# Kernel tuning notes

Hardware: AMD Instinct MI355X
Metric: run time of the kernel (lower is better)

The kernel has to match this reference:

```python
import jax, jax.numpy as jnp
import numpy as np

N, E, F, H = 20000, 320000, 128, 256   # nodes, edges, in-features, hidden
M, NQ = 4096, 2048                      # lsq rows, QP variables
LAMB_MAX = 2.0


def setup_inputs() -> dict:
    key = jax.random.key(0)
    ks = jax.random.split(key, 12)
    x = jax.random.normal(ks[0], (N, F), jnp.float32)
    edge_index = jax.random.randint(ks[1], (2, E), 0, N)
    A = jax.random.normal(ks[2], (M, NQ), jnp.float32) * 0.05
    b = jax.random.normal(ks[3], (M, 1), jnp.float32)
    feat_ids = jax.random.randint(ks[4], (NQ,), 0, N)
    x_prior = jax.random.uniform(ks[5], (NQ, 1), jnp.float32)
    lamb = jnp.ones((1,), jnp.float32)
    # ChebConv K=2 weights: one linear per Chebyshev order, plus bias
    W10 = jax.random.normal(ks[6], (F, H), jnp.float32) / np.sqrt(F)
    W11 = jax.random.normal(ks[7], (F, H), jnp.float32) / np.sqrt(F)
    b1 = jnp.zeros((H,), jnp.float32)
    W20 = jax.random.normal(ks[8], (H, 1), jnp.float32) / np.sqrt(H)
    W21 = jax.random.normal(ks[9], (H, 1), jnp.float32) / np.sqrt(H)
    b2 = jnp.zeros((1,), jnp.float32)
    return {"x": x, "edge_index": edge_index, "A": A, "b": b,
            "feat_ids": feat_ids, "x_prior": x_prior, "lamb": lamb,
            "W10": W10, "W11": W11, "b1": b1,
            "W20": W20, "W21": W21, "b2": b2}


def _cheb_conv(x, edge_index, W0, W1, bias, lam_max):
    """PyG ChebConv with K=2: out = x @ W0 + (2L/lam_max - I) x @ W1 + bias,
    L = I - D^{-1/2} A D^{-1/2}, via edge gather/scatter (no dense NxN)."""
    row, col = edge_index[0], edge_index[1]
    n = x.shape[0]
    deg = jax.ops.segment_sum(jnp.ones_like(row, dtype=x.dtype), row, num_segments=n)
    dinv = jnp.where(deg > 0, deg ** -0.5, 0.0)
    # normalized edge weight scaled by 2/lam_max, negated (off-diag of L_hat)
    w = -(2.0 / lam_max) * dinv[row] * dinv[col]              # [E]
    msg = jax.ops.segment_sum(w[:, None] * x[col], row, num_segments=n)
    Tx1 = msg + (2.0 / lam_max - 1.0) * x                      # diagonal of L_hat
    return x @ W0 + Tx1 @ W1 + bias


def reference(x, edge_index, A, b, feat_ids, x_prior, lamb,
              W10, W11, b1, W20, W21, b2):
    h = jax.nn.relu(_cheb_conv(x, edge_index, W10, W11, b1, LAMB_MAX))
    h = lamb[0] * jax.nn.relu(_cheb_conv(h, edge_index, W20, W21, b2, LAMB_MAX))
    hfold = h[feat_ids] + 1e-5                                 # [NQ, 1]
    q = hfold[:, 0]
    # QP: min 1/2 z^T Q z + p^T z with vacuous inequality (0*z <= 0.1) and no
    # equality constraints -> interior-point converges to unconstrained min.
    Q = A.T @ A + jnp.diag(q)                                  # [NQ, NQ]
    p = -(x_prior * hfold)[:, 0] - (b.T @ A)[0]                # [NQ]
    z = jnp.linalg.solve(Q, -p)                                # [NQ]
    return z[:, None]                                          # f.T -> [NQ, 1]
```

## Files before the change

kernel.cpp:

```cpp
#include <hip/hip_runtime.h>

#define N_NODES 20000
#define N_EDGES 320000
#define F_DIM   128
#define H_DIM   256
#define M_ROWS  4096
#define NQ      2048
#define NIT     18
#define MM_ROWS 20032

typedef __attribute__((ext_vector_type(8))) short short8;
typedef __attribute__((ext_vector_type(4))) float f32x4;


__device__ __forceinline__ float wred(float v) {
#pragma unroll
  for (int m = 32; m > 0; m >>= 1) v += __shfl_xor(v, m, 64);
  return v;
}

__device__ __forceinline__ float bred256(float v, float* lds) {
  v = wred(v);
  int w = threadIdx.x >> 6;
  if ((threadIdx.x & 63) == 0) lds[w] = v;
  __syncthreads();
  float tot = lds[0] + lds[1] + lds[2] + lds[3];
  __syncthreads();
  return tot;
}

__device__ __forceinline__ unsigned f2bf(float f) {
  unsigned u = __float_as_uint(f);
  unsigned r = u + 0x7fffu + ((u >> 16) & 1u);
  return r >> 16;
}
__device__ __forceinline__ float bflo(unsigned u) { return __uint_as_float(u << 16); }
__device__ __forceinline__ float bfhi(unsigned u) { return __uint_as_float(u & 0xffff0000u); }


__global__ __launch_bounds__(256) void k_deg(const int* __restrict__ ei, int* __restrict__ deg) {
  int e = blockIdx.x * 256 + threadIdx.x;
  if (e < N_EDGES) atomicAdd(&deg[ei[e]], 1);
}

__global__ __launch_bounds__(1024) void k_scan(const int* __restrict__ deg,
    int* __restrict__ rowstart, float* __restrict__ dinv) {
  __shared__ int part[1024];
  int t = threadIdx.x;
  const int chunk = (N_NODES + 1023) / 1024;
  int lo = t * chunk;
  int hi = lo + chunk; if (hi > N_NODES) hi = N_NODES;
  int s = 0;
  for (int i = lo; i < hi; ++i) {
    int d = deg[i];
    dinv[i] = d > 0 ? rsqrtf((float)d) : 0.f;
    s += d;
  }
  part[t] = s;
  __syncthreads();
  for (int off = 1; off < 1024; off <<= 1) {
    int v = part[t];
    int add = (t >= off) ? part[t - off] : 0;
    __syncthreads();
    part[t] = v + add;
    __syncthreads();
  }
  int base = (t > 0) ? part[t - 1] : 0;
  for (int i = lo; i < hi; ++i) { rowstart[i] = base; base += deg[i]; }
  if (t == 0) rowstart[N_NODES] = part[1023];
}

__global__ __launch_bounds__(256) void k_scatter(const int* __restrict__ ei,
    const int* __restrict__ rowstart, int* __restrict__ cursor,
    const float* __restrict__ dinv, int* __restrict__ cols, float* __restrict__ wvals) {
  int e = blockIdx.x * 256 + threadIdx.x;
  if (e >= N_EDGES) return;
  int r = ei[e];
  int c = ei[N_EDGES + e];
  int pos = rowstart[r] + atomicAdd(&cursor[r], 1);
  cols[pos] = c;
  wvals[pos] = -dinv[r] * dinv[c];
}

#define CONVX_BLKS (MM_ROWS * 16 / 256)

__global__ __launch_bounds__(256) void k_pack(const float* __restrict__ x,
    const float* __restrict__ W10, const float* __restrict__ W11,
    unsigned* __restrict__ xu, unsigned* __restrict__ Wtb) {
  int bx = blockIdx.x;
  if (bx < CONVX_BLKS) {
    int gid = bx * 256 + threadIdx.x;
    int row = gid >> 4;
    int q8 = gid & 15;
    uint4* xu4 = (uint4*)xu;
    if (row < N_NODES) {
      const float4* x4 = (const float4*)x;
      float4 a = x4[(size_t)row * 32 + q8 * 2];
      float4 b = x4[(size_t)row * 32 + q8 * 2 + 1];
      uint4 u;
      u.x = f2bf(a.x) | (f2bf(a.y) << 16);
      u.y = f2bf(a.z) | (f2bf(a.w) << 16);
      u.z = f2bf(b.x) | (f2bf(b.y) << 16);
      u.w = f2bf(b.z) | (f2bf(b.w) << 16);
      xu4[(size_t)row * 32 + q8] = u;
    } else {
      uint4 z = make_uint4(0, 0, 0, 0);
      xu4[(size_t)row * 32 + q8] = z;
      xu4[(size_t)row * 32 + 16 + q8] = z;
    }
  } else {
    int gid = (bx - CONVX_BLKS) * 256 + threadIdx.x;
    int n = gid >> 7;
    int u = gid & 127;
    int k0 = u * 2;
    float v0 = (k0 < 128) ? W10[(size_t)k0 * H_DIM + n]
                          : W11[(size_t)(k0 - 128) * H_DIM + n];
    float v1 = (k0 + 1 < 128) ? W10[(size_t)(k0 + 1) * H_DIM + n]
                              : W11[(size_t)(k0 - 127) * H_DIM + n];
    Wtb[(size_t)n * 128 + u] = f2bf(v0) | (f2bf(v1) << 16);
  }
}

__global__ __launch_bounds__(256) void k_msg1(const int* __restrict__ rowstart,
    const int* __restrict__ cols, const float* __restrict__ wvals,
    unsigned* __restrict__ xu) {
  int wid = (blockIdx.x * 256 + threadIdx.x) >> 6;
  int lane = threadIdx.x & 63;
  if (wid >= N_NODES) return;
  int s0 = rowstart[wid], s1 = rowstart[wid + 1];
  float2 acc = make_float2(0.f, 0.f);
  for (int e = s0; e < s1; ++e) {
    int c = cols[e];
    float w = wvals[e];
    unsigned u = xu[(size_t)c * 128 + lane];
    acc.x += w * bflo(u);
    acc.y += w * bfhi(u);
  }
  xu[(size_t)wid * 128 + 64 + lane] = f2bf(acc.x) | (f2bf(acc.y) << 16);
}

#define WS_ST 20

__global__ __launch_bounds__(256) void k_mm(const unsigned* __restrict__ xu,
    const unsigned* __restrict__ Wtb, const float* __restrict__ b1,
    const float* __restrict__ W20, const float* __restrict__ W21,
    float* __restrict__ t, float* __restrict__ s) {
  __shared__ unsigned Ws[2][256 * WS_ST];
  const int row0 = blockIdx.x * 64;
  const int tid = threadIdx.x;
  const int w = tid >> 6, lane = tid & 63;
  const int colb = w * 64;
  const int frow = lane & 15, fqo = (lane >> 4) * 4;
  const int c16 = lane & 15, q4 = lane >> 4;

  f32x4 acc[4][4];
#pragma unroll
  for (int a = 0; a < 4; ++a)
#pragma unroll
    for (int b = 0; b < 4; ++b) {
      acc[a][b][0] = 0.f; acc[a][b][1] = 0.f;
      acc[a][b][2] = 0.f; acc[a][b][3] = 0.f;
    }

  const uint4* Wtb4 = (const uint4*)Wtb;
  uint4 rw[4];
#pragma unroll
  for (int j = 0; j < 4; ++j) rw[j] = Wtb4[(size_t)tid * 32 + j];

  for (int kc = 0; kc < 8; ++kc) {
    const int b = kc & 1;
    unsigned* dst = Ws[b] + tid * WS_ST;
#pragma unroll
    for (int j = 0; j < 4; ++j) *(uint4*)(dst + j * 4) = rw[j];
    if (kc + 1 < 8) {
#pragma unroll
      for (int j = 0; j < 4; ++j) rw[j] = Wtb4[(size_t)tid * 32 + (kc + 1) * 4 + j];
    }
    __syncthreads();
    short8 af[4], bf[4];
#pragma unroll
    for (int a = 0; a < 4; ++a)
      af[a] = *(const short8*)(xu + (size_t)(row0 + a * 16 + frow) * 128 + kc * 16 + fqo);
#pragma unroll
    for (int n = 0; n < 4; ++n)
      bf[n] = *(const short8*)(Ws[b] + (colb + n * 16 + frow) * WS_ST + fqo);
#pragma unroll
    for (int a = 0; a < 4; ++a)
#pragma unroll
      for (int n = 0; n < 4; ++n)
        acc[a][n] = __builtin_amdgcn_mfma_f32_16x16x32_bf16(af[a], bf[n], acc[a][n], 0, 0, 0);
    __syncthreads();
  }

  float tp[4][4] = {}, sp[4][4] = {};
#pragma unroll
  for (int b2 = 0; b2 < 4; ++b2) {
    int gc = colb + b2 * 16 + c16;
    float w20 = W20[gc], w21 = W21[gc], bb = b1[gc];
#pragma unroll
    for (int a = 0; a < 4; ++a)
#pragma unroll
      for (int r = 0; r < 4; ++r) {
        float val = acc[a][b2][r] + bb;
        val = val > 0.f ? val : 0.f;
        tp[a][r] += val * w20;
        sp[a][r] += val * w21;
      }
  }
#pragma unroll
  for (int a = 0; a < 4; ++a)
#pragma unroll
    for (int r = 0; r < 4; ++r) {
#pragma unroll
      for (int m = 1; m < 16; m <<= 1) {
        tp[a][r] += __shfl_xor(tp[a][r], m, 64);
        sp[a][r] += __shfl_xor(sp[a][r], m, 64);
      }
    }
  if (c16 == 0) {
#pragma unroll
    for (int a = 0; a < 4; ++a)
#pragma unroll
      for (int r = 0; r < 4; ++r) {
        int gr = row0 + a * 16 + q4 * 4 + r;
        if (gr < N_NODES) {
          atomicAdd(&t[gr], tp[a][r]);
          atomicAdd(&s[gr], sp[a][r]);
        }
      }
  }
}


__global__ __launch_bounds__(256) void k_h2(const float* __restrict__ t,
    const float* __restrict__ s, const int* __restrict__ rowstart,
    const int* __restrict__ cols, const float* __restrict__ wvals,
    const float* __restrict__ lamb, const float* __restrict__ b2, float* __restrict__ h2) {
  int i = blockIdx.x * 256 + threadIdx.x;
  if (i >= N_NODES) return;
  float m = 0.f;
  int s0 = rowstart[i], s1 = rowstart[i + 1];
  for (int e = s0; e < s1; ++e) m += wvals[e] * s[cols[e]];
  float val = t[i] + m + b2[0];
  val = val > 0.f ? val : 0.f;
  h2[i] = lamb[0] * val;
}

__global__ __launch_bounds__(256) void k_prep(const float* __restrict__ A,
    const float* __restrict__ b, unsigned* __restrict__ Atu, float* __restrict__ btA_parts) {
  int jp = blockIdx.x * 256 + threadIdx.x;
  int k0 = blockIdx.y * 128;
  const float2* A2 = (const float2*)A;
  float acc0 = 0.f, acc1 = 0.f;
  for (int kk = 0; kk < 128; kk += 8) {
    float ax[8], ay[8];
#pragma unroll
    for (int i = 0; i < 8; ++i) {
      int k = k0 + kk + i;
      float2 a = A2[(size_t)k * 1024 + jp];
      float bk = b[k];
      acc0 += a.x * bk;
      acc1 += a.y * bk;
      ax[i] = a.x; ay[i] = a.y;
    }
    uint4 t0, t1;
    t0.x = f2bf(ax[0]) | (f2bf(ax[1]) << 16);
    t0.y = f2bf(ax[2]) | (f2bf(ax[3]) << 16);
    t0.z = f2bf(ax[4]) | (f2bf(ax[5]) << 16);
    t0.w = f2bf(ax[6]) | (f2bf(ax[7]) << 16);
    t1.x = f2bf(ay[0]) | (f2bf(ay[1]) << 16);
    t1.y = f2bf(ay[2]) | (f2bf(ay[3]) << 16);
    t1.z = f2bf(ay[4]) | (f2bf(ay[5]) << 16);
    t1.w = f2bf(ay[6]) | (f2bf(ay[7]) << 16);
    int uoff = (k0 + kk) >> 1;
    *(uint4*)(Atu + (size_t)(2 * jp) * 2048 + uoff) = t0;
    *(uint4*)(Atu + (size_t)(2 * jp + 1) * 2048 + uoff) = t1;
  }
  ((float2*)(btA_parts + (size_t)blockIdx.y * NQ))[jp] = make_float2(acc0, acc1);
}

__global__ __launch_bounds__(256) void k_qrhs(const float* __restrict__ h2,
    const int* __restrict__ feat_ids, const float* __restrict__ x_prior,
    const float* __restrict__ btA_parts, float* __restrict__ q, float* __restrict__ r) {
  int j = blockIdx.x * 256 + threadIdx.x;
  int f = feat_ids[j];
  float hf = h2[f] + 1e-5f;
  q[j] = hf;
  float bta = 0.f;
#pragma unroll
  for (int c = 0; c < 32; ++c) bta += btA_parts[(size_t)c * NQ + j];
  r[j] = x_prior[j] * hf + bta;
}

#define GR_ST 20
#define NTILE 136

__global__ __launch_bounds__(512) void k_gram(const unsigned* __restrict__ Atu,
                                              float* __restrict__ Gp) {
  __shared__ unsigned shmem[10240];
  int uu = blockIdx.x, bi = 0;
  while (uu >= 16 - bi) { uu -= 16 - bi; ++bi; }
  const int bj = bi + uu;
  const int i0 = bi * 128, j0 = bj * 128;
  const int kq = blockIdx.y;
  const int tid = threadIdx.x;
  const int grp = tid >> 8;
  const int t8 = tid & 255;
  const int w = tid >> 6;
  const int wt = w & 3;
  const int lane = tid & 63;
  const int wr = (wt >> 1) * 64, wc = (wt & 1) * 64;
  const int srow = t8 >> 1, suo = (t8 & 1) * 8;
  const int frow = lane & 15, fqo = (lane >> 4) * 4;

  unsigned* shA = shmem + grp * 5120;
  unsigned* shB = shA + 2560;

  f32x4 acc[4][4];
#pragma unroll
  for (int a = 0; a < 4; ++a)
#pragma unroll
    for (int b = 0; b < 4; ++b) {
      acc[a][b][0] = 0.f; acc[a][b][1] = 0.f;
      acc[a][b][2] = 0.f; acc[a][b][3] = 0.f;
    }

  const unsigned* pa = Atu + (size_t)(i0 + srow) * 2048 + kq * 512 + suo;
  const unsigned* pb = Atu + (size_t)(j0 + srow) * 2048 + kq * 512 + suo;

  int ku = grp * 16;
  uint4 ra0 = *(const uint4*)(pa + ku);
  uint4 ra1 = *(const uint4*)(pa + ku + 4);
  uint4 rb0 = *(const uint4*)(pb + ku);
  uint4 rb1 = *(const uint4*)(pb + ku + 4);

  for (int si = 0; si < 16; ++si) {
    unsigned* as = shA + srow * GR_ST + suo;
    unsigned* bs = shB + srow * GR_ST + suo;
    *(uint4*)as = ra0; *(uint4*)(as + 4) = ra1;
    *(uint4*)bs = rb0; *(uint4*)(bs + 4) = rb1;
    if (si + 1 < 16) {
      ku = (si + 1) * 32 + grp * 16;
      ra0 = *(const uint4*)(pa + ku);
      ra1 = *(const uint4*)(pa + ku + 4);
      rb0 = *(const uint4*)(pb + ku);
      rb1 = *(const uint4*)(pb + ku + 4);
    }
    __syncthreads();
    short8 af[4], bf[4];
#pragma unroll
    for (int a = 0; a < 4; ++a)
      af[a] = *(const short8*)(shA + (wr + a * 16 + frow) * GR_ST + fqo);
#pragma unroll
    for (int b2 = 0; b2 < 4; ++b2)
      bf[b2] = *(const short8*)(shB + (wc + b2 * 16 + frow) * GR_ST + fqo);
#pragma unroll
    for (int a = 0; a < 4; ++a)
#pragma unroll
      for (int b2 = 0; b2 < 4; ++b2)
        acc[a][b2] = __builtin_amdgcn_mfma_f32_16x16x32_bf16(af[a], bf[b2], acc[a][b2], 0, 0, 0);
    __syncthreads();
  }

  const int q4 = lane >> 4, c16 = lane & 15;
  float* comb = (float*)shmem;
#pragma unroll
  for (int rnd = 0; rnd < 2; ++rnd) {
    if (grp == 1 && (wt >> 1) == rnd) {
      float* dst = comb + (wt & 1) * 4160;
#pragma unroll
      for (int a = 0; a < 4; ++a)
#pragma unroll
        for (int b2 = 0; b2 < 4; ++b2)
#pragma unroll
          for (int r = 0; r < 4; ++r)
            dst[(a * 16 + q4 * 4 + r) * 65 + b2 * 16 + c16] = acc[a][b2][r];
    }
    __syncthreads();
    if (grp == 0 && (wt >> 1) == rnd) {
      const float* src = comb + (wt & 1) * 4160;
#pragma unroll
      for (int a = 0; a < 4; ++a)
#pragma unroll
        for (int b2 = 0; b2 < 4; ++b2)
#pragma unroll
          for (int r = 0; r < 4; ++r)
            acc[a][b2][r] += src[(a * 16 + q4 * 4 + r) * 65 + b2 * 16 + c16];
    }
    __syncthreads();
  }

  if (grp == 0) {
    float* Gz = Gp + ((size_t)kq * NTILE + blockIdx.x) * 16384;
#pragma unroll
    for (int a = 0; a < 4; ++a)
#pragma unroll
      for (int b2 = 0; b2 < 4; ++b2)
#pragma unroll
        for (int r = 0; r < 4; ++r) {
          int lr = wr + a * 16 + q4 * 4 + r;
          int lc = wc + b2 * 16 + c16;
          Gz[lr * 128 + lc] = acc[a][b2][r];
        }
  }
}

#define GT_ST 131

__global__ __launch_bounds__(256) void k_gconv(const float* __restrict__ Gp,
    const float* __restrict__ q, unsigned* __restrict__ Gb, float* __restrict__ qcorr) {
  __shared__ unsigned short T[128 * GT_ST];
  int uu = blockIdx.x, bi = 0;
  while (uu >= 16 - bi) { uu -= 16 - bi; ++bi; }
  const int bj = bi + uu;
  const int tid = threadIdx.x;
  const int r = tid >> 1, ch = (tid & 1) * 64;
  const size_t tile = (size_t)blockIdx.x * 16384;
  const float4* P0 = (const float4*)(Gp + tile + r * 128 + ch);
  const float4* P1 = (const float4*)(Gp + (size_t)1 * NTILE * 16384 + tile + r * 128 + ch);
  const float4* P2 = (const float4*)(Gp + (size_t)2 * NTILE * 16384 + tile + r * 128 + ch);
  const float4* P3 = (const float4*)(Gp + (size_t)3 * NTILE * 16384 + tile + r * 128 + ch);
  const int gr = bi * 128 + r;
  const bool hasdiag = (bi == bj) && (r >= ch) && (r < ch + 64);
  unsigned uo[32];
#pragma unroll
  for (int j = 0; j < 16; ++j) {
    float4 a = P0[j], b = P1[j], c = P2[j], d = P3[j];
    float v0 = a.x + b.x + c.x + d.x;
    float v1 = a.y + b.y + c.y + d.y;
    float v2 = a.z + b.z + c.z + d.z;
    float v3 = a.w + b.w + c.w + d.w;
    const int c0 = ch + j * 4;
    if (hasdiag && (r - c0 >= 0) && (r - c0 < 4)) {
      float qv = q[gr];
      int dsel = r - c0;
      if (dsel == 0) v0 += qv;
      else if (dsel == 1) v1 += qv;
      else if (dsel == 2) v2 += qv;
      else v3 += qv;
      float vd = (dsel == 0) ? v0 : (dsel == 1) ? v1 : (dsel == 2) ? v2 : v3;
      qcorr[gr] = vd - bflo(f2bf(vd));
    }
    unsigned u0 = f2bf(v0) | (f2bf(v1) << 16);
    unsigned u1 = f2bf(v2) | (f2bf(v3) << 16);
    uo[2 * j] = u0;
    uo[2 * j + 1] = u1;
    T[r * GT_ST + c0]     = (unsigned short)(u0 & 0xffffu);
    T[r * GT_ST + c0 + 1] = (unsigned short)(u0 >> 16);
    T[r * GT_ST + c0 + 2] = (unsigned short)(u1 & 0xffffu);
    T[r * GT_ST + c0 + 3] = (unsigned short)(u1 >> 16);
  }
  uint4* dst = (uint4*)(Gb + (size_t)gr * 1024 + bj * 64 + (ch >> 1));
#pragma unroll
  for (int j = 0; j < 8; ++j) dst[j] = ((const uint4*)uo)[j];
  __syncthreads();
  if (bi != bj) {
    const int wv = tid >> 6, lane = tid & 63;
    for (int kk = 0; kk < 32; ++kk) {
      int rr = kk * 4 + wv;
      unsigned lo = T[(2 * lane) * GT_ST + rr];
      unsigned hi = T[(2 * lane + 1) * GT_ST + rr];
      Gb[(size_t)(bj * 128 + rr) * 1024 + bi * 64 + lane] = lo | (hi << 16);
    }
  }
}

__global__ __launch_bounds__(256) void k_cgG(int k, const unsigned* __restrict__ Gb,
    const float* __restrict__ qcorr,
    const float* __restrict__ r_old, float* __restrict__ r_new,
    const float* __restrict__ p_old, float* __restrict__ p_new,
    const float* __restrict__ Qp_in, float* __restrict__ Qp_out,
    float* __restrict__ xcg) {
  __shared__ float pshare[NQ];
  __shared__ float lds[4];
  const int tid = threadIdx.x, bid = blockIdx.x;
  const float4* r4 = (const float4*)r_old;
  float4 ra = r4[tid * 2], rb2 = r4[tid * 2 + 1];
  float pv[8];
  if (k == 0) {
    pv[0] = ra.x; pv[1] = ra.y; pv[2] = ra.z; pv[3] = ra.w;
    pv[4] = rb2.x; pv[5] = rb2.y; pv[6] = rb2.z; pv[7] = rb2.w;
    if (bid == 0) {
      ((float4*)p_new)[tid * 2] = ra;
      ((float4*)p_new)[tid * 2 + 1] = rb2;
    }
  } else {
    const float4* p4 = (const float4*)p_old;
    const float4* qp4 = (const float4*)Qp_in;
    float4 pa = p4[tid * 2], pb = p4[tid * 2 + 1];
    float4 qa = qp4[tid * 2], qb = qp4[tid * 2 + 1];
    float rr = ra.x * ra.x + ra.y * ra.y + ra.z * ra.z + ra.w * ra.w +
               rb2.x * rb2.x + rb2.y * rb2.y + rb2.z * rb2.z + rb2.w * rb2.w;
    float pap = pa.x * qa.x + pa.y * qa.y + pa.z * qa.z + pa.w * qa.w +
                pb.x * qb.x + pb.y * qb.y + pb.z * qb.z + pb.w * qb.w;
    rr = bred256(rr, lds);
    pap = bred256(pap, lds);
    float alpha = rr / pap;
    if (bid == 0) {
      float4* x4 = (float4*)xcg;
      float4 xa = x4[tid * 2], xb = x4[tid * 2 + 1];
      xa.x += alpha * pa.x; xa.y += alpha * pa.y;
      xa.z += alpha * pa.z; xa.w += alpha * pa.w;
      xb.x += alpha * pb.x; xb.y += alpha * pb.y;
      xb.z += alpha * pb.z; xb.w += alpha * pb.w;
      x4[tid * 2] = xa; x4[tid * 2 + 1] = xb;
    }
    ra.x -= alpha * qa.x; ra.y -= alpha * qa.y;
    ra.z -= alpha * qa.z; ra.w -= alpha * qa.w;
    rb2.x -= alpha * qb.x; rb2.y -= alpha * qb.y;
    rb2.z -= alpha * qb.z; rb2.w -= alpha * qb.w;
    float rrn = ra.x * ra.x + ra.y * ra.y + ra.z * ra.z + ra.w * ra.w +
                rb2.x * rb2.x + rb2.y * rb2.y + rb2.z * rb2.z + rb2.w * rb2.w;
    rrn = bred256(rrn, lds);
    float beta = rrn / rr;
    pv[0] = ra.x + beta * pa.x; pv[1] = ra.y + beta * pa.y;
    pv[2] = ra.z + beta * pa.z; pv[3] = ra.w + beta * pa.w;
    pv[4] = rb2.x + beta * pb.x; pv[5] = rb2.y + beta * pb.y;
    pv[6] = rb2.z + beta * pb.z; pv[7] = rb2.w + beta * pb.w;
    if (bid == 0) {
      ((float4*)r_new)[tid * 2] = ra;
      ((float4*)r_new)[tid * 2 + 1] = rb2;
      ((float4*)p_new)[tid * 2] = make_float4(pv[0], pv[1], pv[2], pv[3]);
      ((float4*)p_new)[tid * 2 + 1] = make_float4(pv[4], pv[5], pv[6], pv[7]);
    }
  }
  ((float4*)pshare)[tid * 2] = make_float4(pv[0], pv[1], pv[2], pv[3]);
  ((float4*)pshare)[tid * 2 + 1] = make_float4(pv[4], pv[5], pv[6], pv[7]);
  __syncthreads();
  const int w = tid >> 6, lane = tid & 63;
  const int row = bid * 4 + w;
  const uint4* Gr = (const uint4*)(Gb + (size_t)row * 1024);
  const float4* ps4 = (const float4*)pshare;
  float acc = 0.f;
#pragma unroll
  for (int c = 0; c < 4; ++c) {
    uint4 gv = Gr[c * 64 + lane];
    float4 pa = ps4[c * 128 + lane * 2];
    float4 pb = ps4[c * 128 + lane * 2 + 1];
    acc += bflo(gv.x) * pa.x + bfhi(gv.x) * pa.y;
    acc += bflo(gv.y) * pa.z + bfhi(gv.y) * pa.w;
    acc += bflo(gv.z) * pb.x + bfhi(gv.z) * pb.y;
    acc += bflo(gv.w) * pb.z + bfhi(gv.w) * pb.w;
  }
  acc = wred(acc);
  if (lane == 0) Qp_out[row] = acc + qcorr[row] * pshare[row];
}

__global__ __launch_bounds__(256) void k_cgfin(const float* __restrict__ r_last,
    const float* __restrict__ p_last, const float* __restrict__ Qp,
    const float* __restrict__ xcg, float* __restrict__ out) {
  const int tid = threadIdx.x;
  const int lane = tid & 63;
  const float4* r4 = (const float4*)r_last;
  const float4* p4 = (const float4*)p_last;
  const float4* q4 = (const float4*)Qp;
  float rr = 0.f, pap = 0.f;
#pragma unroll
  for (int c = 0; c < 4; ++c) {
#pragma unroll
    for (int hh = 0; hh < 2; ++hh) {
      float4 rv = r4[c * 128 + lane * 2 + hh];
      float4 pv = p4[c * 128 + lane * 2 + hh];
      float4 qv = q4[c * 128 + lane * 2 + hh];
      rr += rv.x * rv.x + rv.y * rv.y + rv.z * rv.z + rv.w * rv.w;
      pap += pv.x * qv.x + pv.y * qv.y + pv.z * qv.z + pv.w * qv.w;
    }
  }
  rr = wred(rr);
  pap = wred(pap);
  float alpha = rr / pap;
  const float4* x4 = (const float4*)xcg;
  float4* o4 = (float4*)out;
#pragma unroll
  for (int hh = 0; hh < 2; ++hh) {
    int i4 = tid * 2 + hh;
    float4 xv = x4[i4];
    float4 pv = p4[i4];
    xv.x += alpha * pv.x; xv.y += alpha * pv.y;
    xv.z += alpha * pv.z; xv.w += alpha * pv.w;
    o4[i4] = xv;
  }
}


extern "C" void kernel_launch(void* const* d_in, const int* in_sizes, int n_in,
                              void* d_out, int out_size, void* d_ws, size_t ws_size,
                              hipStream_t stream) {
  const float* x      = (const float*)d_in[0];
  const int*   ei     = (const int*)d_in[1];
  const float* A      = (const float*)d_in[2];
  const float* b      = (const float*)d_in[3];
  const int*   fids   = (const int*)d_in[4];
  const float* xprior = (const float*)d_in[5];
  const float* lamb   = (const float*)d_in[6];
  const float* W10    = (const float*)d_in[7];
  const float* W11    = (const float*)d_in[8];
  const float* b1     = (const float*)d_in[9];
  const float* W20    = (const float*)d_in[10];
  const float* W21    = (const float*)d_in[11];
  const float* b2     = (const float*)d_in[12];
  float* out = (float*)d_out;

  char* base = (char*)d_ws;
  size_t o = 0;
  auto alloc = [&](size_t bytes) { size_t r = o; o = (o + bytes + 255) & ~size_t(255); return r; };

  size_t off_deg    = alloc(N_NODES * 4);
  size_t off_cursor = alloc(N_NODES * 4);
  size_t off_xcg    = alloc(NQ * 4);
  size_t off_t      = alloc(N_NODES * 4);
  size_t off_s      = alloc(N_NODES * 4);
  size_t zero_end   = o;
  size_t off_rowst  = alloc((N_NODES + 1) * 4);
  size_t off_dinv   = alloc(N_NODES * 4);
  size_t off_h2     = alloc(N_NODES * 4);
  size_t off_q      = alloc(NQ * 4);
  size_t off_r0     = alloc(NQ * 4);
  size_t off_r1     = alloc(NQ * 4);
  size_t off_p0     = alloc(NQ * 4);
  size_t off_p1     = alloc(NQ * 4);
  size_t off_Qp0    = alloc(NQ * 4);
  size_t off_Qp1    = alloc(NQ * 4);
  size_t off_qcorr  = alloc(NQ * 4);
  size_t off_btAp   = alloc(32 * NQ * 4);
  size_t off_Wtb    = alloc(256 * 128 * 4);
  size_t sz_cols  = (size_t)N_EDGES * 4 + 256;
  size_t sz_wvals = (size_t)N_EDGES * 4 + 256;
  size_t sz_xmsg  = (size_t)MM_ROWS * 256 * 2;
  size_t union_gnn = sz_cols + sz_wvals + sz_xmsg;
  size_t union_at  = (size_t)M_ROWS * NQ * 2;
  size_t off_union = alloc(union_gnn > union_at ? union_gnn : union_at);
  size_t off_Gp    = alloc((size_t)4 * NTILE * 16384 * 4);
  if (o > ws_size) return;

  int*   deg      = (int*)(base + off_deg);
  int*   cursor   = (int*)(base + off_cursor);
  float* xcg      = (float*)(base + off_xcg);
  float* t        = (float*)(base + off_t);
  float* s        = (float*)(base + off_s);
  int*   rowstart = (int*)(base + off_rowst);
  float* dinv     = (float*)(base + off_dinv);
  float* h2       = (float*)(base + off_h2);
  float* q        = (float*)(base + off_q);
  float* rb[2]    = {(float*)(base + off_r0), (float*)(base + off_r1)};
  float* pg[2]    = {(float*)(base + off_p0), (float*)(base + off_p1)};
  float* Qpb[2]   = {(float*)(base + off_Qp0), (float*)(base + off_Qp1)};
  float* qcorr    = (float*)(base + off_qcorr);
  float* btA_parts = (float*)(base + off_btAp);
  unsigned* Wtb   = (unsigned*)(base + off_Wtb);
  int*   cols     = (int*)(base + off_union);
  float* wvals    = (float*)(base + off_union + sz_cols);
  unsigned* xmsgb = (unsigned*)(base + off_union + sz_cols + sz_wvals);
  unsigned* Atu   = (unsigned*)(base + off_union);
  unsigned* Gb    = (unsigned*)(base + off_union);
  float* Gp       = (float*)(base + off_Gp);

  hipMemsetAsync(d_ws, 0, zero_end, stream);

  k_deg<<<(N_EDGES + 255) / 256, 256, 0, stream>>>(ei, deg);
  k_scan<<<1, 1024, 0, stream>>>(deg, rowstart, dinv);
  k_scatter<<<(N_EDGES + 255) / 256, 256, 0, stream>>>(ei, rowstart, cursor, dinv, cols, wvals);

  k_pack<<<CONVX_BLKS + 128, 256, 0, stream>>>(x, W10, W11, xmsgb, Wtb);
  k_msg1<<<N_NODES / 4, 256, 0, stream>>>(rowstart, cols, wvals, xmsgb);
  k_mm<<<MM_ROWS / 64, 256, 0, stream>>>(xmsgb, Wtb, b1, W20, W21, t, s);
  k_h2<<<(N_NODES + 255) / 256, 256, 0, stream>>>(t, s, rowstart, cols, wvals, lamb, b2, h2);

  k_prep<<<dim3(4, 32), 256, 0, stream>>>(A, b, Atu, btA_parts);
  k_qrhs<<<NQ / 256, 256, 0, stream>>>(h2, fids, xprior, btA_parts, q, rb[0]);
  k_gram<<<dim3(NTILE, 4), 512, 0, stream>>>(Atu, Gp);
  k_gconv<<<NTILE, 256, 0, stream>>>(Gp, q, Gb, qcorr);

  k_cgG<<<512, 256, 0, stream>>>(0, Gb, qcorr, rb[0], rb[0], pg[0], pg[0],
                                 Qpb[1], Qpb[0], xcg);
  for (int k = 1; k < NIT; ++k) {
    k_cgG<<<512, 256, 0, stream>>>(k, Gb, qcorr, rb[(k - 1) & 1], rb[k & 1],
                                   pg[(k - 1) & 1], pg[k & 1],
                                   Qpb[(k - 1) & 1], Qpb[k & 1], xcg);
  }
  k_cgfin<<<1, 256, 0, stream>>>(rb[(NIT - 1) & 1], pg[(NIT - 1) & 1],
                                 Qpb[(NIT - 1) & 1], xcg, out);
}
```

Baseline: 415.1 us.

## Load k_mm fragments directly from global and simplify k_gram to single-group blocks

k_mm drops its LDS staging of the weight tile and its barriers. It now loads A and B MFMA fragments straight from global memory, double-buffered in registers across k-chunks. k_gram moves from 512-thread blocks, where two halves split the K range and combined results through LDS, to 256-thread blocks that each run the full 512-column K slice. The grid is remapped to a 1D launch with an XCD-aware swizzle of tile and kq. The aim is to remove intra-block reduction and sync overhead and improve L2 locality, at the cost of more global fragment loads and fewer waves per block.

```diff
diff --git a/kernel.cpp b/kernel.cpp
--- a/kernel.cpp
+++ b/kernel.cpp
@@ -139,13 +139,21 @@
   xu[(size_t)wid * 128 + 64 + lane] = f2bf(acc.x) | (f2bf(acc.y) << 16);
 }
 
-#define WS_ST 20
+
+__device__ __forceinline__ void mm_ldfrag(short8* Af, short8* Bf,
+    const unsigned* __restrict__ xurow, const unsigned* __restrict__ wrow, int kc) {
+#pragma unroll
+  for (int a = 0; a < 4; ++a)
+    Af[a] = *(const short8*)(xurow + (size_t)a * 16 * 128 + kc * 16);
+#pragma unroll
+  for (int n = 0; n < 4; ++n)
+    Bf[n] = *(const short8*)(wrow + (size_t)n * 16 * 128 + kc * 16);
+}
 
 __global__ __launch_bounds__(256) void k_mm(const unsigned* __restrict__ xu,
     const unsigned* __restrict__ Wtb, const float* __restrict__ b1,
     const float* __restrict__ W20, const float* __restrict__ W21,
     float* __restrict__ t, float* __restrict__ s) {
-  __shared__ unsigned Ws[2][256 * WS_ST];
   const int row0 = blockIdx.x * 64;
   const int tid = threadIdx.x;
   const int w = tid >> 6, lane = tid & 63;
@@ -162,34 +170,26 @@
       acc[a][b][2] = 0.f; acc[a][b][3] = 0.f;
     }
 
-  const uint4* Wtb4 = (const uint4*)Wtb;
-  uint4 rw[4];
-#pragma unroll
-  for (int j = 0; j < 4; ++j) rw[j] = Wtb4[(size_t)tid * 32 + j];
-
-  for (int kc = 0; kc < 8; ++kc) {
-    const int b = kc & 1;
-    unsigned* dst = Ws[b] + tid * WS_ST;
-#pragma unroll
-    for (int j = 0; j < 4; ++j) *(uint4*)(dst + j * 4) = rw[j];
-    if (kc + 1 < 8) {
-#pragma unroll
-      for (int j = 0; j < 4; ++j) rw[j] = Wtb4[(size_t)tid * 32 + (kc + 1) * 4 + j];
-    }
-    __syncthreads();
-    short8 af[4], bf[4];
+  const unsigned* xurow = xu + (size_t)(row0 + frow) * 128 + fqo;
+  const unsigned* wrow  = Wtb + (size_t)(colb + frow) * 128 + fqo;
+
+  short8 A0[4], B0[4], A1[4], B1[4];
+  mm_ldfrag(A0, B0, xurow, wrow, 0);
+#pragma unroll
+  for (int kp = 0; kp < 4; ++kp) {
+    const int kc = kp * 2;
+    mm_ldfrag(A1, B1, xurow, wrow, kc + 1);
 #pragma unroll
     for (int a = 0; a < 4; ++a)
-      af[a] = *(const short8*)(xu + (size_t)(row0 + a * 16 + frow) * 128 + kc * 16 + fqo);
-#pragma unroll
-    for (int n = 0; n < 4; ++n)
-      bf[n] = *(const short8*)(Ws[b] + (colb + n * 16 + frow) * WS_ST + fqo);
+#pragma unroll
+      for (int n = 0; n < 4; ++n)
+        acc[a][n] = __builtin_amdgcn_mfma_f32_16x16x32_bf16(A0[a], B0[n], acc[a][n], 0, 0, 0);
+    if (kc + 2 < 8) mm_ldfrag(A0, B0, xurow, wrow, kc + 2);
 #pragma unroll
     for (int a = 0; a < 4; ++a)
 #pragma unroll
       for (int n = 0; n < 4; ++n)
-        acc[a][n] = __builtin_amdgcn_mfma_f32_16x16x32_bf16(af[a], bf[n], acc[a][n], 0, 0, 0);
-    __syncthreads();
+        acc[a][n] = __builtin_amdgcn_mfma_f32_16x16x32_bf16(A1[a], B1[n], acc[a][n], 0, 0, 0);
   }
 
   float tp[4][4] = {}, sp[4][4] = {};
@@ -295,26 +295,23 @@
 #define GR_ST 20
 #define NTILE 136
 
-__global__ __launch_bounds__(512) void k_gram(const unsigned* __restrict__ Atu,
+__global__ __launch_bounds__(256) void k_gram(const unsigned* __restrict__ Atu,
                                               float* __restrict__ Gp) {
-  __shared__ unsigned shmem[10240];
-  int uu = blockIdx.x, bi = 0;
+  __shared__ unsigned shA[128 * GR_ST];
+  __shared__ unsigned shB[128 * GR_ST];
+  const int bid = blockIdx.x;
+  const int wid = (bid & 7) * 68 + (bid >> 3);
+  const int tile = wid >> 2;
+  const int kq = wid & 3;
+  int uu = tile, bi = 0;
   while (uu >= 16 - bi) { uu -= 16 - bi; ++bi; }
   const int bj = bi + uu;
   const int i0 = bi * 128, j0 = bj * 128;
-  const int kq = blockIdx.y;
   const int tid = threadIdx.x;
-  const int grp = tid >> 8;
-  const int t8 = tid & 255;
-  const int w = tid >> 6;
-  const int wt = w & 3;
-  const int lane = tid & 63;
-  const int wr = (wt >> 1) * 64, wc = (wt & 1) * 64;
-  const int srow = t8 >> 1, suo = (t8 & 1) * 8;
+  const int w = tid >> 6, lane = tid & 63;
+  const int wr = (w >> 1) * 64, wc = (w & 1) * 64;
+  const int srow = tid >> 1, suo = (tid & 1) * 8;
   const int frow = lane & 15, fqo = (lane >> 4) * 4;
-
-  unsigned* shA = shmem + grp * 5120;
-  unsigned* shB = shA + 2560;
 
   f32x4 acc[4][4];
 #pragma unroll
@@ -328,19 +325,19 @@
   const unsigned* pa = Atu + (size_t)(i0 + srow) * 2048 + kq * 512 + suo;
   const unsigned* pb = Atu + (size_t)(j0 + srow) * 2048 + kq * 512 + suo;
 
-  int ku = grp * 16;
-  uint4 ra0 = *(const uint4*)(pa + ku);
-  uint4 ra1 = *(const uint4*)(pa + ku + 4);
-  uint4 rb0 = *(const uint4*)(pb + ku);
-  uint4 rb1 = *(const uint4*)(pb + ku + 4);
-
-  for (int si = 0; si < 16; ++si) {
-    unsigned* as = shA + srow * GR_ST + suo;
-    unsigned* bs = shB + srow * GR_ST + suo;
+  uint4 ra0 = *(const uint4*)(pa);
+  uint4 ra1 = *(const uint4*)(pa + 4);
+  uint4 rb0 = *(const uint4*)(pb);
+  uint4 rb1 = *(const uint4*)(pb + 4);
+
+  unsigned* as = shA + srow * GR_ST + suo;
+  unsigned* bs = shB + srow * GR_ST + suo;
+
+  for (int si = 0; si < 32; ++si) {
     *(uint4*)as = ra0; *(uint4*)(as + 4) = ra1;
     *(uint4*)bs = rb0; *(uint4*)(bs + 4) = rb1;
-    if (si + 1 < 16) {
-      ku = (si + 1) * 32 + grp * 16;
+    if (si + 1 < 32) {
+      const int ku = (si + 1) * 16;
       ra0 = *(const uint4*)(pa + ku);
       ra1 = *(const uint4*)(pa + ku + 4);
       rb0 = *(const uint4*)(pb + ku);
@@ -363,46 +360,17 @@
   }
 
   const int q4 = lane >> 4, c16 = lane & 15;
-  float* comb = (float*)shmem;
-#pragma unroll
-  for (int rnd = 0; rnd < 2; ++rnd) {
-    if (grp == 1 && (wt >> 1) == rnd) {
-      float* dst = comb + (wt & 1) * 4160;
-#pragma unroll
-      for (int a = 0; a < 4; ++a)
-#pragma unroll
-        for (int b2 = 0; b2 < 4; ++b2)
-#pragma unroll
-          for (int r = 0; r < 4; ++r)
-            dst[(a * 16 + q4 * 4 + r) * 65 + b2 * 16 + c16] = acc[a][b2][r];
-    }
-    __syncthreads();
-    if (grp == 0 && (wt >> 1) == rnd) {
-      const float* src = comb + (wt & 1) * 4160;
-#pragma unroll
-      for (int a = 0; a < 4; ++a)
-#pragma unroll
-        for (int b2 = 0; b2 < 4; ++b2)
-#pragma unroll
-          for (int r = 0; r < 4; ++r)
-            acc[a][b2][r] += src[(a * 16 + q4 * 4 + r) * 65 + b2 * 16 + c16];
-    }
-    __syncthreads();
-  }
-
-  if (grp == 0) {
-    float* Gz = Gp + ((size_t)kq * NTILE + blockIdx.x) * 16384;
-#pragma unroll
-    for (int a = 0; a < 4; ++a)
-#pragma unroll
-      for (int b2 = 0; b2 < 4; ++b2)
-#pragma unroll
-        for (int r = 0; r < 4; ++r) {
-          int lr = wr + a * 16 + q4 * 4 + r;
-          int lc = wc + b2 * 16 + c16;
-          Gz[lr * 128 + lc] = acc[a][b2][r];
-        }
-  }
+  float* Gz = Gp + ((size_t)kq * NTILE + tile) * 16384;
+#pragma unroll
+  for (int a = 0; a < 4; ++a)
+#pragma unroll
+    for (int b2 = 0; b2 < 4; ++b2)
+#pragma unroll
+      for (int r = 0; r < 4; ++r) {
+        int lr = wr + a * 16 + q4 * 4 + r;
+        int lc = wc + b2 * 16 + c16;
+        Gz[lr * 128 + lc] = acc[a][b2][r];
+      }
 }
 
 #define GT_ST 131
@@ -668,7 +636,7 @@
 
   k_prep<<<dim3(4, 32), 256, 0, stream>>>(A, b, Atu, btA_parts);
   k_qrhs<<<NQ / 256, 256, 0, stream>>>(h2, fids, xprior, btA_parts, q, rb[0]);
-  k_gram<<<dim3(NTILE, 4), 512, 0, stream>>>(Atu, Gp);
+  k_gram<<<544, 256, 0, stream>>>(Atu, Gp);
   k_gconv<<<NTILE, 256, 0, stream>>>(Gp, q, Gb, qcorr);
 
   k_cgG<<<512, 256, 0, stream>>>(0, Gb, qcorr, rb[0], rb[0], pg[0], pg[0],
```

Measured after the change: 403.7 us. 1.03x faster.
